# Kernel tuning notes

Measured on AMD Instinct MI355X. Metric: run time of the kernel, lower is better.

## Reference

```python
import jax, jax.numpy as jnp
import numpy as np

D = 196; NCH = 64; H = 8; DH = 64; INNER = H * DH; MLP = 784; SEQ = 65


def _ln(x, g, b, eps=1e-5):
    m = x.mean(-1, keepdims=True)
    v = x.var(-1, keepdims=True)
    return (x - m) / jnp.sqrt(v + eps) * g + b


def setup_inputs() -> dict:
    key = jax.random.key(0)
    ks = jax.random.split(key, 12)
    f = jax.random.normal
    return dict(
        x=f(ks[0], (1, SEQ, D), dtype=jnp.float32),
        tokens=f(ks[1], (1, D), dtype=jnp.float32),
        x_pe=f(ks[2], (1, NCH, D), dtype=jnp.float32),
        conv_k=f(ks[3], (3, 3), dtype=jnp.float32) * 0.3,   # Conv2d(1,1,3) kernel
        bn_g=jnp.ones(()), bn_b=jnp.zeros(()), bn_rm=jnp.zeros(()), bn_rv=jnp.ones(()),
        fc_w1=f(ks[4], (NCH, 12)) * 0.1,
        fc_w2=f(ks[5], (12, NCH)) * 0.1,
        ln1_g=jnp.ones((D,)), ln1_b=jnp.zeros((D,)),
        ln2_g=jnp.ones((D,)), ln2_b=jnp.zeros((D,)),
        w_qkv=f(ks[6], (D, 3 * INNER)) * 0.05,
        w_out=f(ks[7], (INNER, D)) * 0.05, b_out=jnp.zeros((D,)),
        ff_w1=f(ks[8], (D, MLP)) * 0.05, ff_b1=jnp.zeros((MLP,)),
        ff_w2=f(ks[9], (MLP, D)) * 0.05, ff_b2=jnp.zeros((D,)),
    )


def reference(x, tokens, x_pe, conv_k, bn_g, bn_b, bn_rm, bn_rv,
              fc_w1, fc_w2, ln1_g, ln1_b, ln2_g, ln2_b,
              w_qkv, w_out, b_out, ff_w1, ff_b1, ff_w2, ff_b2):
    # --- per-channel Conv2d(1,1,3,p=1)+BN+ReLU, batched over all 64 rows ---
    # Each row is (1,1,1,196): height 1 with pad 1 means the top/bottom kernel
    # rows only touch zero padding, so only the middle kernel row contributes
    # -> equivalent to a 1D conv with kernel conv_k[1].
    rows = x_pe[0]                      # [64,196]
    km = conv_k[1]                      # [3]
    xp = jnp.pad(rows, ((0, 0), (1, 1)))
    conv = km[0] * xp[:, :D] + km[1] * xp[:, 1:D + 1] + km[2] * xp[:, 2:D + 2]
    bn = (conv - bn_rm) / jnp.sqrt(bn_rv + 1e-5) * bn_g + bn_b
    a = jax.nn.relu(bn)                 # [64,196]  (== x_AfterConv / a)

    # --- sort-based suppress/excitation channel gating ---
    b1 = a.mean(-1)                     # [64] adaptive avg pool
    val = jnp.sort(b1)
    idx = jnp.argsort(b1)
    middle = jnp.where((val.max() < 0) | (val.min() > 0),
                       jnp.int32(32), jnp.argmax(val > 0).astype(jnp.int32))
    rank = jnp.argsort(idx)             # rank of each channel in ascending order
    sup = rank < middle                 # channels in idx[:middle]
    l_s = middle.astype(b1.dtype)
    l_e = (NCH - middle).astype(b1.dtype)
    b2 = jnp.where(sup,
                   b1 - 1.0 / (1.0 + jnp.power(l_s, b1)),
                   b1 + 1.0 / (1.0 + jnp.power(l_e, -b1)))

    c = jax.nn.sigmoid(jax.nn.relu(b2 @ fc_w1) @ fc_w2)   # [64]
    x_att = a * c[:, None]                                  # [64,196]
    x_att = jnp.concatenate([x_att, tokens.reshape(1, D)], axis=0)[None]  # [1,65,196]

    # --- PreNorm attention ---
    h = _ln(x, ln1_g, ln1_b)
    qkv = h @ w_qkv
    q, k, v = jnp.split(qkv, 3, axis=-1)
    def heads(t):
        return t.reshape(1, SEQ, H, DH).transpose(0, 2, 1, 3)  # b h n d
    q, k, v = heads(q), heads(k), heads(v)
    attn = jax.nn.softmax(jnp.einsum('bhnd,bhmd->bhnm', q, k) * (DH ** -0.5), axis=-1)
    o = jnp.einsum('bhnm,bhmd->bhnd', attn, v).transpose(0, 2, 1, 3).reshape(1, SEQ, INNER)
    x = o @ w_out + b_out + x + x_att

    # --- PreNorm feed-forward ---
    h2 = _ln(x, ln2_g, ln2_b)
    x = (jax.nn.gelu(h2 @ ff_w1 + ff_b1, approximate=False) @ ff_w2 + ff_b2) + x
    return x
```

## Files before the change

kernel.cpp:

```cpp
#include <hip/hip_runtime.h>
#include <math.h>

#define D 196
#define NCH 64
#define NH 8
#define DHD 64
#define INNER 512
#define MLP 784
#define SEQ 65

__device__ __forceinline__ float bsum(float v, float* red) {
    for (int off = 32; off > 0; off >>= 1) v += __shfl_down(v, off, 64);
    int lane = threadIdx.x & 63, wid = threadIdx.x >> 6;
    if (lane == 0) red[wid] = v;
    __syncthreads();
    float s = red[0] + red[1] + red[2] + red[3];
    __syncthreads();
    return s;
}

__global__ void __launch_bounds__(256) k1(const float* __restrict__ x_pe,
        const float* __restrict__ conv_k, const float* __restrict__ bn_g,
        const float* __restrict__ bn_b, const float* __restrict__ bn_rm,
        const float* __restrict__ bn_rv, const float* __restrict__ x,
        const float* __restrict__ ln1_g, const float* __restrict__ ln1_b,
        const float* __restrict__ w_qkv,
        float* __restrict__ a, float* __restrict__ b1, float* __restrict__ qkv,
        float* __restrict__ out) {
    __shared__ float red[4];
    __shared__ float h[D];
    __shared__ float ps[512];
    int b = blockIdx.x, t = threadIdx.x;
    if (b < NCH) {
        int zi = b * 200 + t;
        if (t < 200 && zi < SEQ * D) out[zi] = 0.f;
        const float* row = x_pe + b * D;
        float val = 0.f;
        if (t < D) {
            float km0 = conv_k[3], km1 = conv_k[4], km2 = conv_k[5];
            float inv = rsqrtf(bn_rv[0] + 1e-5f);
            float l = (t > 0) ? row[t - 1] : 0.f;
            float m = row[t];
            float r = (t < D - 1) ? row[t + 1] : 0.f;
            float conv = km0 * l + km1 * m + km2 * r;
            float bn = (conv - bn_rm[0]) * inv * bn_g[0] + bn_b[0];
            val = fmaxf(bn, 0.f);
            a[b * D + t] = val;
        }
        float tot = bsum(val, red);
        if (t == 0) b1[b] = tot * (1.f / (float)D);
    } else {
        int qb = b - NCH;
        int n = qb / 12, cg = qb % 12;
        const float* row = x + n * D;
        float v = (t < D) ? row[t] : 0.f;
        float mean = bsum(v, red) * (1.f / (float)D);
        float d = (t < D) ? (v - mean) : 0.f;
        float var = bsum(d * d, red) * (1.f / (float)D);
        float rinv = rsqrtf(var + 1e-5f);
        if (t < D) h[t] = d * rinv * ln1_g[t] + ln1_b[t];
        __syncthreads();
        int qq = t >> 6, lt = t & 63;
        int c0 = cg * 128 + lt * 2;
        const float* wp = w_qkv + (qq * 49) * 1536 + c0;
        const float* hp = h + qq * 49;
        float a0 = 0.f, a1 = 0.f;
#pragma unroll
        for (int i = 0; i < 49; i++) {
            float2 w2 = *(const float2*)(wp + i * 1536);
            float hv = hp[i];
            a0 += hv * w2.x;
            a1 += hv * w2.y;
        }
        ps[qq * 128 + lt * 2] = a0;
        ps[qq * 128 + lt * 2 + 1] = a1;
        __syncthreads();
        if (t < 64) {
            float s0 = ps[t * 2] + ps[128 + t * 2] + ps[256 + t * 2] + ps[384 + t * 2];
            float s1 = ps[t * 2 + 1] + ps[129 + t * 2] + ps[257 + t * 2] + ps[385 + t * 2];
            float2 o2 = make_float2(s0, s1);
            *(float2*)(qkv + n * 1536 + cg * 128 + t * 2) = o2;
        }
    }
}

__global__ void __launch_bounds__(512) k2(const float* __restrict__ b1,
        const float* __restrict__ fc_w1, const float* __restrict__ fc_w2,
        const float* __restrict__ qkv, const float* __restrict__ w_out,
        const float* __restrict__ b_out, const float* __restrict__ x,
        float* __restrict__ c, float* __restrict__ x2) {
    int b = blockIdx.x, t = threadIdx.x;
    if (b == SEQ) {
        __shared__ float sb1[NCH];
        __shared__ float sb2[NCH];
        __shared__ float hid[12];
        if (t < NCH) sb1[t] = b1[t];
        __syncthreads();
        if (t < NCH) {
            float v = sb1[t];
            float mx = -1e30f, mn = 1e30f;
            int cle = 0, rank = 0;
            for (int j = 0; j < NCH; j++) {
                float w = sb1[j];
                mx = fmaxf(mx, w);
                mn = fminf(mn, w);
                if (w <= 0.f) cle++;
                if (w < v || (w == v && j < t)) rank++;
            }
            int middle;
            if (mx < 0.f || mn > 0.f) middle = 32;
            else if (mx <= 0.f) middle = 0;
            else middle = cle;
            float b2;
            if (rank < middle) {
                float ls = (float)middle;
                b2 = v - 1.f / (1.f + powf(ls, v));
            } else {
                float le = (float)(NCH - middle);
                b2 = v + 1.f / (1.f + powf(le, -v));
            }
            sb2[t] = b2;
        }
        __syncthreads();
        if (t < 12) {
            float s = 0.f;
            for (int j = 0; j < NCH; j++) s += sb2[j] * fc_w1[j * 12 + t];
            hid[t] = fmaxf(s, 0.f);
        }
        __syncthreads();
        if (t < NCH) {
            float s = 0.f;
            for (int k = 0; k < 12; k++) s += hid[k] * fc_w2[k * NCH + t];
            c[t] = 1.f / (1.f + expf(-s));
        }
        return;
    }
    __shared__ float sq[512];
    __shared__ float pp[8 * 80];
    __shared__ float so[512];
    __shared__ float ps[784];
    int n = b;
    int w = t >> 6, L = t & 63;
    sq[t] = qkv[n * 1536 + t];
    __syncthreads();
    const float scale = 0.125f;
    const float4* kr = (const float4*)(qkv + L * 1536 + INNER + w * DHD);
    const float4* q4 = (const float4*)(sq + w * DHD);
    float s = 0.f;
#pragma unroll
    for (int i = 0; i < 16; i++) {
        float4 kv = kr[i];
        float4 qv = q4[i];
        s += qv.x * kv.x + qv.y * kv.y + qv.z * kv.z + qv.w * kv.w;
    }
    float sL = s * scale;
    float t64 = sq[w * DHD + L] * qkv[64 * 1536 + INNER + w * DHD + L];
#pragma unroll
    for (int off = 1; off < 64; off <<= 1) t64 += __shfl_xor(t64, off, 64);
    float s64 = t64 * scale;
    float mx = sL;
#pragma unroll
    for (int off = 1; off < 64; off <<= 1) mx = fmaxf(mx, __shfl_xor(mx, off, 64));
    mx = fmaxf(mx, s64);
    float e = expf(sL - mx);
    float e64 = expf(s64 - mx);
    float esum = e;
#pragma unroll
    for (int off = 1; off < 64; off <<= 1) esum += __shfl_xor(esum, off, 64);
    esum += e64;
    float rs = 1.f / esum;
    pp[w * 80 + L] = e;
    if (L == 0) pp[w * 80 + 64] = e64;
    __syncthreads();
    float acc = 0.f;
#pragma unroll 13
    for (int m = 0; m < SEQ; m++)
        acc += pp[w * 80 + m] * qkv[m * 1536 + 2 * INNER + w * DHD + L];
    so[w * DHD + L] = acc * rs;
    __syncthreads();
    if (t < 392) {
        int qq = t / 98, p = t - qq * 98;
        const float* wp = w_out + (qq * 128) * D + 2 * p;
        const float* op = so + qq * 128;
        float a0 = 0.f, a1 = 0.f;
#pragma unroll 16
        for (int i = 0; i < 128; i++) {
            float2 w2 = *(const float2*)(wp + i * D);
            float ov = op[i];
            a0 += ov * w2.x;
            a1 += ov * w2.y;
        }
        ps[qq * 196 + 2 * p] = a0;
        ps[qq * 196 + 2 * p + 1] = a1;
    }
    __syncthreads();
    if (t < 98) {
        float s0 = ps[2 * t] + ps[196 + 2 * t] + ps[392 + 2 * t] + ps[588 + 2 * t];
        float s1 = ps[2 * t + 1] + ps[197 + 2 * t] + ps[393 + 2 * t] + ps[589 + 2 * t];
        float2 xr = *(const float2*)(x + n * D + 2 * t);
        float2 br = *(const float2*)(b_out + 2 * t);
        float2 o2 = make_float2(s0 + xr.x + br.x, s1 + xr.y + br.y);
        *(float2*)(x2 + n * D + 2 * t) = o2;
    }
}

__global__ void __launch_bounds__(256) k3(const float* __restrict__ x2,
        const float* __restrict__ a, const float* __restrict__ c,
        const float* __restrict__ tokens,
        const float* __restrict__ ln2_g, const float* __restrict__ ln2_b,
        const float* __restrict__ ff_w1, const float* __restrict__ ff_b1,
        float* __restrict__ tb) {
    __shared__ float red[4];
    __shared__ float h[D];
    __shared__ float ps[392];
    int n = blockIdx.x, cg = blockIdx.y, t = threadIdx.x;
    float v = 0.f;
    if (t < D) {
        float att = (n < NCH) ? a[n * D + t] * c[n] : tokens[t];
        v = x2[n * D + t] + att;
    }
    float mean = bsum(v, red) * (1.f / (float)D);
    float d = (t < D) ? (v - mean) : 0.f;
    float var = bsum(d * d, red) * (1.f / (float)D);
    float rinv = rsqrtf(var + 1e-5f);
    if (t < D) h[t] = d * rinv * ln2_g[t] + ln2_b[t];
    __syncthreads();
    if (t < D) {
        int qq = t / 49, p = t - qq * 49;
        int c0 = cg * 98 + 2 * p;
        const float* wp = ff_w1 + (qq * 49) * MLP + c0;
        const float* hp = h + qq * 49;
        float a0 = 0.f, a1 = 0.f;
#pragma unroll
        for (int i = 0; i < 49; i++) {
            float2 w2 = *(const float2*)(wp + i * MLP);
            float hv = hp[i];
            a0 += hv * w2.x;
            a1 += hv * w2.y;
        }
        if (qq == 0) { a0 += ff_b1[c0]; a1 += ff_b1[c0 + 1]; }
        ps[qq * 98 + 2 * p] = a0;
        ps[qq * 98 + 2 * p + 1] = a1;
    }
    __syncthreads();
    if (t < 49) {
        float s0 = ps[2 * t] + ps[98 + 2 * t] + ps[196 + 2 * t] + ps[294 + 2 * t];
        float s1 = ps[2 * t + 1] + ps[99 + 2 * t] + ps[197 + 2 * t] + ps[295 + 2 * t];
        float g0 = 0.5f * s0 * (1.f + erff(s0 * 0.70710678118f));
        float g1 = 0.5f * s1 * (1.f + erff(s1 * 0.70710678118f));
        *(float2*)(tb + n * MLP + cg * 98 + 2 * t) = make_float2(g0, g1);
    }
}

__global__ void __launch_bounds__(256) k4(const float* __restrict__ tb,
        const float* __restrict__ ff_w2, const float* __restrict__ ff_b2,
        const float* __restrict__ x2, const float* __restrict__ a,
        const float* __restrict__ c, const float* __restrict__ tokens,
        float* __restrict__ out) {
    __shared__ float st[98];
    __shared__ float ps[392];
    int n = blockIdx.x, kc = blockIdx.y, t = threadIdx.x;
    if (t < 98) st[t] = tb[n * MLP + kc * 98 + t];
    __syncthreads();
    if (t < D) {
        int hh = t / 98, p = t - hh * 98;
        const float* wp = ff_w2 + (kc * 98 + hh * 49) * D + 2 * p;
        const float* sp = st + hh * 49;
        float a0 = 0.f, a1 = 0.f;
#pragma unroll
        for (int i = 0; i < 49; i++) {
            float2 w2 = *(const float2*)(wp + i * D);
            float sv = sp[i];
            a0 += sv * w2.x;
            a1 += sv * w2.y;
        }
        ps[hh * 196 + 2 * p] = a0;
        ps[hh * 196 + 2 * p + 1] = a1;
    }
    __syncthreads();
    if (t < 98) {
        float s0 = ps[2 * t] + ps[196 + 2 * t];
        float s1 = ps[2 * t + 1] + ps[197 + 2 * t];
        if (kc == 0) {
            int c0 = 2 * t;
            float att0 = (n < NCH) ? a[n * D + c0] * c[n] : tokens[c0];
            float att1 = (n < NCH) ? a[n * D + c0 + 1] * c[n] : tokens[c0 + 1];
            s0 += ff_b2[c0] + x2[n * D + c0] + att0;
            s1 += ff_b2[c0 + 1] + x2[n * D + c0 + 1] + att1;
        }
        atomicAdd(&out[n * D + 2 * t], s0);
        atomicAdd(&out[n * D + 2 * t + 1], s1);
    }
}

extern "C" void kernel_launch(void* const* d_in, const int* in_sizes, int n_in,
                              void* d_out, int out_size, void* d_ws, size_t ws_size,
                              hipStream_t stream) {
    const float* x      = (const float*)d_in[0];
    const float* tokens = (const float*)d_in[1];
    const float* x_pe   = (const float*)d_in[2];
    const float* conv_k = (const float*)d_in[3];
    const float* bn_g   = (const float*)d_in[4];
    const float* bn_b   = (const float*)d_in[5];
    const float* bn_rm  = (const float*)d_in[6];
    const float* bn_rv  = (const float*)d_in[7];
    const float* fc_w1  = (const float*)d_in[8];
    const float* fc_w2  = (const float*)d_in[9];
    const float* ln1_g  = (const float*)d_in[10];
    const float* ln1_b  = (const float*)d_in[11];
    const float* ln2_g  = (const float*)d_in[12];
    const float* ln2_b  = (const float*)d_in[13];
    const float* w_qkv  = (const float*)d_in[14];
    const float* w_out  = (const float*)d_in[15];
    const float* b_out  = (const float*)d_in[16];
    const float* ff_w1  = (const float*)d_in[17];
    const float* ff_b1  = (const float*)d_in[18];
    const float* ff_w2  = (const float*)d_in[19];
    const float* ff_b2  = (const float*)d_in[20];
    float* out = (float*)d_out;

    float* ws = (float*)d_ws;
    float* a    = ws;
    float* b1   = ws + 12544;
    float* cc   = ws + 12608;
    float* qkv  = ws + 12672;
    float* x2   = ws + 112512;
    float* tb   = ws + 125252;

    k1<<<844, 256, 0, stream>>>(x_pe, conv_k, bn_g, bn_b, bn_rm, bn_rv,
                                x, ln1_g, ln1_b, w_qkv, a, b1, qkv, out);
    k2<<<SEQ + 1, 512, 0, stream>>>(b1, fc_w1, fc_w2, qkv, w_out, b_out, x, cc, x2);
    k3<<<dim3(SEQ, 8), 256, 0, stream>>>(x2, a, cc, tokens, ln2_g, ln2_b,
                                         ff_w1, ff_b1, tb);
    k4<<<dim3(SEQ, 8), 256, 0, stream>>>(tb, ff_w2, ff_b2, x2, a, cc, tokens, out);
}
```

Before: 132.7 us.

## Fuse gating, attention output, LayerNorm and MLP into one per-token kernel

Merges k2, k3 and k4 into one kernel launched with one 512-thread block per token. Each block recomputes the channel-gating scalar redundantly and keeps x2 and the GELU activations in shared memory. This removes two launches, the global round trips for x2 and tb, the zeroing of out, and the atomic accumulation. In exchange, only 65 blocks each stream the full ff_w1 and ff_w2 serially, so per-block parallelism drops sharply compared with the 520-block grids used before.

```diff
diff --git a/kernel.cpp b/kernel.cpp
--- a/kernel.cpp
+++ b/kernel.cpp
@@ -19,21 +19,28 @@
     return s;
 }
 
+__device__ __forceinline__ float bsum8(float v, float* red) {
+    for (int off = 32; off > 0; off >>= 1) v += __shfl_down(v, off, 64);
+    int lane = threadIdx.x & 63, wid = threadIdx.x >> 6;
+    if (lane == 0) red[wid] = v;
+    __syncthreads();
+    float s = red[0] + red[1] + red[2] + red[3] + red[4] + red[5] + red[6] + red[7];
+    __syncthreads();
+    return s;
+}
+
 __global__ void __launch_bounds__(256) k1(const float* __restrict__ x_pe,
         const float* __restrict__ conv_k, const float* __restrict__ bn_g,
         const float* __restrict__ bn_b, const float* __restrict__ bn_rm,
         const float* __restrict__ bn_rv, const float* __restrict__ x,
         const float* __restrict__ ln1_g, const float* __restrict__ ln1_b,
         const float* __restrict__ w_qkv,
-        float* __restrict__ a, float* __restrict__ b1, float* __restrict__ qkv,
-        float* __restrict__ out) {
+        float* __restrict__ a, float* __restrict__ b1, float* __restrict__ qkv) {
     __shared__ float red[4];
     __shared__ float h[D];
     __shared__ float ps[512];
     int b = blockIdx.x, t = threadIdx.x;
     if (b < NCH) {
-        int zi = b * 200 + t;
-        if (t < 200 && zi < SEQ * D) out[zi] = 0.f;
         const float* row = x_pe + b * D;
         float val = 0.f;
         if (t < D) {
@@ -88,62 +95,70 @@
         const float* __restrict__ fc_w1, const float* __restrict__ fc_w2,
         const float* __restrict__ qkv, const float* __restrict__ w_out,
         const float* __restrict__ b_out, const float* __restrict__ x,
-        float* __restrict__ c, float* __restrict__ x2) {
-    int b = blockIdx.x, t = threadIdx.x;
-    if (b == SEQ) {
-        __shared__ float sb1[NCH];
-        __shared__ float sb2[NCH];
-        __shared__ float hid[12];
-        if (t < NCH) sb1[t] = b1[t];
-        __syncthreads();
-        if (t < NCH) {
-            float v = sb1[t];
-            float mx = -1e30f, mn = 1e30f;
-            int cle = 0, rank = 0;
-            for (int j = 0; j < NCH; j++) {
-                float w = sb1[j];
-                mx = fmaxf(mx, w);
-                mn = fminf(mn, w);
-                if (w <= 0.f) cle++;
-                if (w < v || (w == v && j < t)) rank++;
-            }
-            int middle;
-            if (mx < 0.f || mn > 0.f) middle = 32;
-            else if (mx <= 0.f) middle = 0;
-            else middle = cle;
-            float b2;
-            if (rank < middle) {
-                float ls = (float)middle;
-                b2 = v - 1.f / (1.f + powf(ls, v));
-            } else {
-                float le = (float)(NCH - middle);
-                b2 = v + 1.f / (1.f + powf(le, -v));
-            }
-            sb2[t] = b2;
-        }
-        __syncthreads();
-        if (t < 12) {
-            float s = 0.f;
-            for (int j = 0; j < NCH; j++) s += sb2[j] * fc_w1[j * 12 + t];
-            hid[t] = fmaxf(s, 0.f);
-        }
-        __syncthreads();
-        if (t < NCH) {
-            float s = 0.f;
-            for (int k = 0; k < 12; k++) s += hid[k] * fc_w2[k * NCH + t];
-            c[t] = 1.f / (1.f + expf(-s));
-        }
-        return;
-    }
+        const float* __restrict__ a, const float* __restrict__ tokens,
+        const float* __restrict__ ln2_g, const float* __restrict__ ln2_b,
+        const float* __restrict__ ff_w1, const float* __restrict__ ff_b1,
+        const float* __restrict__ ff_w2, const float* __restrict__ ff_b2,
+        float* __restrict__ out) {
+    __shared__ float red[8];
     __shared__ float sq[512];
     __shared__ float pp[8 * 80];
     __shared__ float so[512];
     __shared__ float ps[784];
-    int n = b;
+    __shared__ float x2row[D];
+    __shared__ float h2[D];
+    __shared__ float tbs[MLP];
+    __shared__ float sb1[NCH];
+    __shared__ float sb2[NCH];
+    __shared__ float hid[12];
+    __shared__ float cgate;
+
+    int n = blockIdx.x, t = threadIdx.x;
+
+    sq[t] = qkv[n * 1536 + t];
+    if (t < NCH) sb1[t] = b1[t];
+    __syncthreads();
+    if (t < NCH) {
+        float v = sb1[t];
+        float mx = -1e30f, mn = 1e30f;
+        int cle = 0, rank = 0;
+        for (int j = 0; j < NCH; j++) {
+            float w = sb1[j];
+            mx = fmaxf(mx, w);
+            mn = fminf(mn, w);
+            if (w <= 0.f) cle++;
+            if (w < v || (w == v && j < t)) rank++;
+        }
+        int middle;
+        if (mx < 0.f || mn > 0.f) middle = 32;
+        else if (mx <= 0.f) middle = 0;
+        else middle = cle;
+        float b2;
+        if (rank < middle) {
+            float ls = (float)middle;
+            b2 = v - 1.f / (1.f + powf(ls, v));
+        } else {
+            float le = (float)(NCH - middle);
+            b2 = v + 1.f / (1.f + powf(le, -v));
+        }
+        sb2[t] = b2;
+    }
+    __syncthreads();
+    if (t < 12) {
+        float s = 0.f;
+        for (int j = 0; j < NCH; j++) s += sb2[j] * fc_w1[j * 12 + t];
+        hid[t] = fmaxf(s, 0.f);
+    }
+    __syncthreads();
+    if (t == 0 && n < NCH) {
+        float s = 0.f;
+        for (int k = 0; k < 12; k++) s += hid[k] * fc_w2[k * NCH + n];
+        cgate = 1.f / (1.f + expf(-s));
+    }
+    __syncthreads();
+
+    const float scale = 0.125f;
     int w = t >> 6, L = t & 63;
-    sq[t] = qkv[n * 1536 + t];
-    __syncthreads();
-    const float scale = 0.125f;
     const float4* kr = (const float4*)(qkv + L * 1536 + INNER + w * DHD);
     const float4* q4 = (const float4*)(sq + w * DHD);
     float s = 0.f;
@@ -178,6 +193,7 @@
         acc += pp[w * 80 + m] * qkv[m * 1536 + 2 * INNER + w * DHD + L];
     so[w * DHD + L] = acc * rs;
     __syncthreads();
+
     if (t < 392) {
         int qq = t / 98, p = t - qq * 98;
         const float* wp = w_out + (qq * 128) * D + 2 * p;
@@ -199,97 +215,66 @@
         float s1 = ps[2 * t + 1] + ps[197 + 2 * t] + ps[393 + 2 * t] + ps[589 + 2 * t];
         float2 xr = *(const float2*)(x + n * D + 2 * t);
         float2 br = *(const float2*)(b_out + 2 * t);
-        float2 o2 = make_float2(s0 + xr.x + br.x, s1 + xr.y + br.y);
-        *(float2*)(x2 + n * D + 2 * t) = o2;
-    }
-}
-
-__global__ void __launch_bounds__(256) k3(const float* __restrict__ x2,
-        const float* __restrict__ a, const float* __restrict__ c,
-        const float* __restrict__ tokens,
-        const float* __restrict__ ln2_g, const float* __restrict__ ln2_b,
-        const float* __restrict__ ff_w1, const float* __restrict__ ff_b1,
-        float* __restrict__ tb) {
-    __shared__ float red[4];
-    __shared__ float h[D];
-    __shared__ float ps[392];
-    int n = blockIdx.x, cg = blockIdx.y, t = threadIdx.x;
-    float v = 0.f;
+        x2row[2 * t] = s0 + xr.x + br.x;
+        x2row[2 * t + 1] = s1 + xr.y + br.y;
+    }
+    __syncthreads();
+
     if (t < D) {
-        float att = (n < NCH) ? a[n * D + t] * c[n] : tokens[t];
-        v = x2[n * D + t] + att;
-    }
-    float mean = bsum(v, red) * (1.f / (float)D);
+        float att = (n < NCH) ? a[n * D + t] * cgate : tokens[t];
+        x2row[t] += att;
+    }
+    __syncthreads();
+
+    float v = (t < D) ? x2row[t] : 0.f;
+    float mean = bsum8(v, red) * (1.f / (float)D);
     float d = (t < D) ? (v - mean) : 0.f;
-    float var = bsum(d * d, red) * (1.f / (float)D);
+    float var = bsum8(d * d, red) * (1.f / (float)D);
     float rinv = rsqrtf(var + 1e-5f);
-    if (t < D) h[t] = d * rinv * ln2_g[t] + ln2_b[t];
-    __syncthreads();
-    if (t < D) {
-        int qq = t / 49, p = t - qq * 49;
-        int c0 = cg * 98 + 2 * p;
-        const float* wp = ff_w1 + (qq * 49) * MLP + c0;
-        const float* hp = h + qq * 49;
+    if (t < D) h2[t] = d * rinv * ln2_g[t] + ln2_b[t];
+    __syncthreads();
+
+    if (t < 392) {
+        int c0 = 2 * t;
+        const float* wp = ff_w1 + c0;
         float a0 = 0.f, a1 = 0.f;
-#pragma unroll
-        for (int i = 0; i < 49; i++) {
+#pragma unroll 4
+        for (int i = 0; i < D; i++) {
             float2 w2 = *(const float2*)(wp + i * MLP);
-            float hv = hp[i];
+            float hv = h2[i];
             a0 += hv * w2.x;
             a1 += hv * w2.y;
         }
-        if (qq == 0) { a0 += ff_b1[c0]; a1 += ff_b1[c0 + 1]; }
-        ps[qq * 98 + 2 * p] = a0;
-        ps[qq * 98 + 2 * p + 1] = a1;
-    }
-    __syncthreads();
-    if (t < 49) {
-        float s0 = ps[2 * t] + ps[98 + 2 * t] + ps[196 + 2 * t] + ps[294 + 2 * t];
-        float s1 = ps[2 * t + 1] + ps[99 + 2 * t] + ps[197 + 2 * t] + ps[295 + 2 * t];
-        float g0 = 0.5f * s0 * (1.f + erff(s0 * 0.70710678118f));
-        float g1 = 0.5f * s1 * (1.f + erff(s1 * 0.70710678118f));
-        *(float2*)(tb + n * MLP + cg * 98 + 2 * t) = make_float2(g0, g1);
-    }
-}
-
-__global__ void __launch_bounds__(256) k4(const float* __restrict__ tb,
-        const float* __restrict__ ff_w2, const float* __restrict__ ff_b2,
-        const float* __restrict__ x2, const float* __restrict__ a,
-        const float* __restrict__ c, const float* __restrict__ tokens,
-        float* __restrict__ out) {
-    __shared__ float st[98];
-    __shared__ float ps[392];
-    int n = blockIdx.x, kc = blockIdx.y, t = threadIdx.x;
-    if (t < 98) st[t] = tb[n * MLP + kc * 98 + t];
-    __syncthreads();
-    if (t < D) {
-        int hh = t / 98, p = t - hh * 98;
-        const float* wp = ff_w2 + (kc * 98 + hh * 49) * D + 2 * p;
-        const float* sp = st + hh * 49;
+        a0 += ff_b1[c0];
+        a1 += ff_b1[c0 + 1];
+        tbs[c0] = 0.5f * a0 * (1.f + erff(a0 * 0.70710678118f));
+        tbs[c0 + 1] = 0.5f * a1 * (1.f + erff(a1 * 0.70710678118f));
+    }
+    __syncthreads();
+
+    if (t < 392) {
+        int qq = t / 98, p = t - qq * 98;
+        const float* wp = ff_w2 + (qq * 196) * D + 2 * p;
+        const float* sp = tbs + qq * 196;
         float a0 = 0.f, a1 = 0.f;
-#pragma unroll
-        for (int i = 0; i < 49; i++) {
+#pragma unroll 4
+        for (int i = 0; i < 196; i++) {
             float2 w2 = *(const float2*)(wp + i * D);
             float sv = sp[i];
             a0 += sv * w2.x;
             a1 += sv * w2.y;
         }
-        ps[hh * 196 + 2 * p] = a0;
-        ps[hh * 196 + 2 * p + 1] = a1;
+        ps[qq * 196 + 2 * p] = a0;
+        ps[qq * 196 + 2 * p + 1] = a1;
     }
     __syncthreads();
     if (t < 98) {
-        float s0 = ps[2 * t] + ps[196 + 2 * t];
-        float s1 = ps[2 * t + 1] + ps[197 + 2 * t];
-        if (kc == 0) {
-            int c0 = 2 * t;
-            float att0 = (n < NCH) ? a[n * D + c0] * c[n] : tokens[c0];
-            float att1 = (n < NCH) ? a[n * D + c0 + 1] * c[n] : tokens[c0 + 1];
-            s0 += ff_b2[c0] + x2[n * D + c0] + att0;
-            s1 += ff_b2[c0 + 1] + x2[n * D + c0 + 1] + att1;
-        }
-        atomicAdd(&out[n * D + 2 * t], s0);
-        atomicAdd(&out[n * D + 2 * t + 1], s1);
+        float s0 = ps[2 * t] + ps[196 + 2 * t] + ps[392 + 2 * t] + ps[588 + 2 * t];
+        float s1 = ps[2 * t + 1] + ps[197 + 2 * t] + ps[393 + 2 * t] + ps[589 + 2 * t];
+        float2 br = *(const float2*)(ff_b2 + 2 * t);
+        float2 o2 = make_float2(s0 + br.x + x2row[2 * t],
+                                s1 + br.y + x2row[2 * t + 1]);
+        *(float2*)(out + n * D + 2 * t) = o2;
     }
 }
 
@@ -322,15 +307,11 @@
     float* ws = (float*)d_ws;
     float* a    = ws;
     float* b1   = ws + 12544;
-    float* cc   = ws + 12608;
-    float* qkv  = ws + 12672;
-    float* x2   = ws + 112512;
-    float* tb   = ws + 125252;
+    float* qkv  = ws + 12608;
 
     k1<<<844, 256, 0, stream>>>(x_pe, conv_k, bn_g, bn_b, bn_rm, bn_rv,
-                                x, ln1_g, ln1_b, w_qkv, a, b1, qkv, out);
-    k2<<<SEQ + 1, 512, 0, stream>>>(b1, fc_w1, fc_w2, qkv, w_out, b_out, x, cc, x2);
-    k3<<<dim3(SEQ, 8), 256, 0, stream>>>(x2, a, cc, tokens, ln2_g, ln2_b,
-                                         ff_w1, ff_b1, tb);
-    k4<<<dim3(SEQ, 8), 256, 0, stream>>>(tb, ff_w2, ff_b2, x2, a, cc, tokens, out);
-}
+                                x, ln1_g, ln1_b, w_qkv, a, b1, qkv);
+    k2<<<SEQ, 512, 0, stream>>>(b1, fc_w1, fc_w2, qkv, w_out, b_out, x,
+                                a, tokens, ln2_g, ln2_b,
+                                ff_w1, ff_b1, ff_w2, ff_b2, out);
+}
```

Measured after the change: 160.4 us. +20.8%, slower.
